# Kernel optimization log

Measured on AMD Instinct MI355X. Metric: run time of the kernel, lower is better.

Reference implementation:

```python
import jax, jax.numpy as jnp
import numpy as np
import math

B, N, C, H, DC = 1, 320, 128, 4, 32  # batch, residues, pair channels, heads, per-head dim


def setup_inputs() -> dict:
    key = jax.random.key(0)
    ks = jax.random.split(key, 8)
    s = lambda k, shape: jax.random.normal(k, shape, dtype=jnp.float32) * 0.02
    return {
        "x2d": jax.random.normal(ks[0], (B, N, N, C), dtype=jnp.float32),
        "mask": jnp.ones((B, N, N), dtype=jnp.float32),
        "ln_g": jnp.ones((C,), jnp.float32),
        "ln_b": jnp.zeros((C,), jnp.float32),
        "wq": s(ks[1], (C, H * DC)),
        "wk": s(ks[2], (C, H * DC)),
        "wv": s(ks[3], (C, H * DC)),
        "wb": s(ks[4], (C, H)),
        "wg": s(ks[5], (C, H * DC)),
        "bg": jnp.zeros((H * DC,), jnp.float32),
        "wo": s(ks[6], (H * DC, C)),
        "bo": jnp.zeros((C,), jnp.float32),
    }


def reference(x2d, mask, ln_g, ln_b, wq, wk, wv, wb, wg, bg, wo, bo):
    # ending_node = False -> no transpose
    # LayerNorm (torch uses biased variance, eps=1e-5)
    mu = x2d.mean(-1, keepdims=True)
    var = ((x2d - mu) ** 2).mean(-1, keepdims=True)
    xn = (x2d - mu) * jax.lax.rsqrt(var + 1e-5) * ln_g + ln_b  # [B,N,N,C]

    sh = xn.shape[:-1]  # (B, N, N)
    q = (xn @ wq).reshape(*sh, H, DC)
    k = (xn @ wk).reshape(*sh, H, DC)
    v = (xn @ wv).reshape(*sh, H, DC)

    scale = 1.0 / math.sqrt(DC)
    aff = jnp.einsum('bmihc,bmjhc->bmhij', q * scale, k)  # [B,N,H,N,N]

    # pair bias: [B,I,J,H] -> [B,1,H,I,J], broadcast over the row axis m
    bterm = jnp.einsum('bijc,ch->bhij', xn, wb)[:, None]
    mask_bias = (100000.0 * (mask - 1.0))[:, :, None, None, :]  # [B,N,1,1,N]

    weights = jax.nn.softmax(aff + bterm + mask_bias, axis=-1)

    g = jax.nn.sigmoid((xn @ wg + bg).reshape(*sh, H, DC))
    out = jnp.einsum('bmhqk,bmkhc->bmqhc', weights, v) * g  # [B,N,N,H,DC]
    out = out.reshape(*sh, H * DC) @ wo + bo  # [B,N,N,C]
    return out
```

## Files before the change

### kernel.cpp

```cpp
#include <hip/hip_runtime.h>
#include <hip/hip_bf16.h>

typedef __attribute__((ext_vector_type(8))) short bf16x8;
typedef __attribute__((ext_vector_type(4))) float f32x4;
typedef __attribute__((ext_vector_type(4))) unsigned short u16x4;

#define DEVI static __device__ __forceinline__

DEVI float bf2f(unsigned short u) {
    union { unsigned int ui; float f; } c; c.ui = ((unsigned int)u) << 16; return c.f;
}
DEVI unsigned short f2bf(float f) {
    union { float f; unsigned int ui; } c; c.f = f;
    unsigned int u = c.ui;
    u += 0x7FFFu + ((u >> 16) & 1u);
    return (unsigned short)(u >> 16);
}
DEVI unsigned int pk2bf(float a, float b) {
    union { __hip_bfloat162 h; unsigned int u; } c;
    c.h = __float22bfloat162_rn(make_float2(a, b));
    return c.u;
}

#define NRES 320
#define NN   102400
#define CCH  128
#define NPAD 328

#define LOG2E 1.4426950408889634f
#define QSCALE (0.17677669529663687f * 1.4426950408889634f)

__global__ __launch_bounds__(256) void k_ln_bias(
    const float* __restrict__ x2d, const float* __restrict__ ln_g,
    const float* __restrict__ ln_b, const float* __restrict__ wb,
    unsigned short* __restrict__ xn, float* __restrict__ bterm)
{
    int wave = threadIdx.x >> 6, lane = threadIdx.x & 63;
    int r = blockIdx.x * 4 + wave;
    int c0 = lane * 2;
    float2 x = *(const float2*)(x2d + (size_t)r * CCH + c0);
    float s = x.x + x.y, sq = x.x * x.x + x.y * x.y;
    #pragma unroll
    for (int m = 1; m < 64; m <<= 1) { s += __shfl_xor(s, m, 64); sq += __shfl_xor(sq, m, 64); }
    float mu = s * (1.0f / 128.0f);
    float var = sq * (1.0f / 128.0f) - mu * mu;
    float rstd = rsqrtf(var + 1e-5f);
    float xn0 = (x.x - mu) * rstd * ln_g[c0] + ln_b[c0];
    float xn1 = (x.y - mu) * rstd * ln_g[c0 + 1] + ln_b[c0 + 1];
    *(unsigned int*)(xn + (size_t)r * CCH + c0) = pk2bf(xn0, xn1);
    float4 w0 = *(const float4*)(wb + c0 * 4);
    float4 w1 = *(const float4*)(wb + c0 * 4 + 4);
    float b0 = xn0 * w0.x + xn1 * w1.x;
    float b1 = xn0 * w0.y + xn1 * w1.y;
    float b2 = xn0 * w0.z + xn1 * w1.z;
    float b3 = xn0 * w0.w + xn1 * w1.w;
    #pragma unroll
    for (int m = 1; m < 64; m <<= 1) {
        b0 += __shfl_xor(b0, m, 64); b1 += __shfl_xor(b1, m, 64);
        b2 += __shfl_xor(b2, m, 64); b3 += __shfl_xor(b3, m, 64);
    }
    if (lane == 0) {
        bterm[0 * NN + r] = b0 * LOG2E; bterm[1 * NN + r] = b1 * LOG2E;
        bterm[2 * NN + r] = b2 * LOG2E; bterm[3 * NN + r] = b3 * LOG2E;
    }
}

__global__ __launch_bounds__(256) void k_proj(
    const unsigned short* __restrict__ xn,
    const float* __restrict__ wq, const float* __restrict__ wk,
    const float* __restrict__ wv, const float* __restrict__ wg,
    const float* __restrict__ bg,
    unsigned short* __restrict__ qkvg)
{
    __shared__ unsigned short A[128][136];
    __shared__ unsigned short Bt[128][136];
    int m0 = blockIdx.x * 128;
    int nt = blockIdx.y;
    int t = threadIdx.x;
    const float* wsrc = (nt == 0) ? wq : (nt == 1) ? wk : (nt == 2) ? wv : wg;
    #pragma unroll
    for (int it = 0; it < 8; ++it) {
        int idx = it * 256 + t;
        int row = idx >> 4, chunk = idx & 15;
        *(bf16x8*)(&A[row][chunk * 8]) = *(const bf16x8*)(xn + (size_t)(m0 + row) * CCH + chunk * 8);
    }
    {
        int n = t & 127, p = t >> 7;
        const float* col = wsrc + n;
        #pragma unroll
        for (int q = 0; q < 8; ++q) {
            int k0 = p * 64 + q * 8;
            union { unsigned int u[4]; bf16x8 v; } pk;
            #pragma unroll
            for (int z = 0; z < 4; ++z)
                pk.u[z] = pk2bf(col[(size_t)(k0 + 2 * z) * 128], col[(size_t)(k0 + 2 * z + 1) * 128]);
            *(bf16x8*)(&Bt[n][k0]) = pk.v;
        }
    }
    __syncthreads();
    int wave = t >> 6, lane = t & 63;
    int wr = (wave >> 1) * 64, wc = (wave & 1) * 64;
    int li = lane & 15, lk = (lane >> 4) * 8;
    f32x4 acc[4][4] = {};
    #pragma unroll
    for (int kk = 0; kk < 4; ++kk) {
        bf16x8 af[4], bfr[4];
        #pragma unroll
        for (int i = 0; i < 4; ++i) af[i] = *(const bf16x8*)(&A[wr + i * 16 + li][kk * 32 + lk]);
        #pragma unroll
        for (int j = 0; j < 4; ++j) bfr[j] = *(const bf16x8*)(&Bt[wc + j * 16 + li][kk * 32 + lk]);
        __builtin_amdgcn_s_setprio(1);
        #pragma unroll
        for (int i = 0; i < 4; ++i)
            #pragma unroll
            for (int j = 0; j < 4; ++j)
                acc[i][j] = __builtin_amdgcn_mfma_f32_16x16x32_bf16(af[i], bfr[j], acc[i][j], 0, 0, 0);
        __builtin_amdgcn_s_setprio(0);
    }
    int rbase = (lane >> 4) * 4;
    bool isg = (nt == 3), isq = (nt == 0);
    #pragma unroll
    for (int i = 0; i < 4; ++i) {
        #pragma unroll
        for (int j = 0; j < 4; ++j) {
            int col = wc + j * 16 + li;
            int gcol = nt * 128 + col;
            #pragma unroll
            for (int r = 0; r < 4; ++r) {
                int grow = m0 + wr + i * 16 + rbase + r;
                float v = acc[i][j][r];
                if (isg) { v += bg[col]; v = 1.0f / (1.0f + __expf(-v)); }
                if (isq) v *= QSCALE;
                qkvg[(size_t)grow * 512 + gcol] = f2bf(v);
            }
        }
    }
}

__global__ __launch_bounds__(256) void k_attn(
    const unsigned short* __restrict__ qkvg,
    const float* __restrict__ bterm,
    const float* __restrict__ mask,
    unsigned short* __restrict__ opre)
{
    __shared__ unsigned short Kl[320][40];
    __shared__ unsigned short VT[32][NPAD];
    __shared__ float mb[320];
    int bid = blockIdx.x;
    int m = bid >> 2, h = bid & 3;
    int t = threadIdx.x;
    size_t base = (size_t)m * NRES * 512;
    for (int idx = t; idx < NRES * 4; idx += 256) {
        int row = idx >> 2, q = idx & 3;
        *(bf16x8*)(&Kl[row][q * 8]) =
            *(const bf16x8*)(qkvg + base + (size_t)row * 512 + 128 + h * 32 + q * 8);
    }
    {
        int dc = t & 31, jg = t >> 5;
        #pragma unroll 8
        for (int jj = 0; jj < 40; jj += 2) {
            int j = jg * 40 + jj;
            unsigned short v0 = qkvg[base + (size_t)j * 512 + 256 + h * 32 + dc];
            unsigned short v1 = qkvg[base + (size_t)(j + 1) * 512 + 256 + h * 32 + dc];
            *(unsigned int*)(&VT[dc][j]) = (unsigned int)v0 | ((unsigned int)v1 << 16);
        }
    }
    for (int j = t; j < NRES; j += 256) mb[j] = (100000.0f * LOG2E) * (mask[(size_t)m * NRES + j] - 1.0f);
    __syncthreads();

    int wave = t >> 6, lane = t & 63;
    int li = lane & 15, lg = lane >> 4;
    int selhi = lg >> 1;
    int srcA = li + ((lane & 16) << 1);
    int srcB = srcA + 16;
    for (int c = 0; c < 5; ++c) {
        int i = wave * 80 + c * 16 + li;
        size_t qrow = base + (size_t)i * 512;
        bf16x8 qf = *(const bf16x8*)(qkvg + qrow + h * 32 + lg * 8);
        const float* brow = bterm + (size_t)h * NN + (size_t)i * NRES;
        f32x4 z = {0.f, 0.f, 0.f, 0.f};
        float mrun = -3.0e38f, sum = 0.0f;
        f32x4 o0 = z, o1 = z;
        float4 bb0 = *(const float4*)(brow + lg * 4);
        float4 bb1 = *(const float4*)(brow + 16 + lg * 4);
        float4 bb2 = *(const float4*)(brow + 32 + lg * 4);
        float4 bb3 = *(const float4*)(brow + 48 + lg * 4);
        #pragma unroll 1
        for (int ph = 0; ph < 5; ++ph) {
            f32x4 st[4];
            #pragma unroll
            for (int jf = 0; jf < 4; ++jf) {
                bf16x8 kf = *(const bf16x8*)(&Kl[ph * 64 + jf * 16 + li][lg * 8]);
                st[jf] = __builtin_amdgcn_mfma_f32_16x16x32_bf16(kf, qf, z, 0, 0, 0);
            }
            float4 bn0, bn1, bn2, bn3;
            if (ph < 4) {
                const float* bnx = brow + (ph + 1) * 64 + lg * 4;
                bn0 = *(const float4*)(bnx);
                bn1 = *(const float4*)(bnx + 16);
                bn2 = *(const float4*)(bnx + 32);
                bn3 = *(const float4*)(bnx + 48);
            }
            float mx = mrun;
            #pragma unroll
            for (int jf = 0; jf < 4; ++jf) {
                int j0 = ph * 64 + jf * 16 + lg * 4;
                float4 mm = *(const float4*)(&mb[j0]);
                float4 bb = (jf == 0) ? bb0 : (jf == 1) ? bb1 : (jf == 2) ? bb2 : bb3;
                st[jf][0] += bb.x + mm.x;
                st[jf][1] += bb.y + mm.y;
                st[jf][2] += bb.z + mm.z;
                st[jf][3] += bb.w + mm.w;
                mx = fmaxf(mx, fmaxf(fmaxf(st[jf][0], st[jf][1]), fmaxf(st[jf][2], st[jf][3])));
            }
            mx = fmaxf(mx, __shfl_xor(mx, 16, 64));
            mx = fmaxf(mx, __shfl_xor(mx, 32, 64));
            if (ph) {
                float corr = __builtin_amdgcn_exp2f(mrun - mx);
                sum *= corr;
                #pragma unroll
                for (int r = 0; r < 4; ++r) { o0[r] *= corr; o1[r] *= corr; }
            }
            mrun = mx;
            #pragma unroll
            for (int w = 0; w < 2; ++w) {
                int jfA = w * 2, jfB = w * 2 + 1;
                float e0 = __builtin_amdgcn_exp2f(st[jfA][0] - mx);
                float e1 = __builtin_amdgcn_exp2f(st[jfA][1] - mx);
                float e2 = __builtin_amdgcn_exp2f(st[jfA][2] - mx);
                float e3 = __builtin_amdgcn_exp2f(st[jfA][3] - mx);
                float f0 = __builtin_amdgcn_exp2f(st[jfB][0] - mx);
                float f1 = __builtin_amdgcn_exp2f(st[jfB][1] - mx);
                float f2 = __builtin_amdgcn_exp2f(st[jfB][2] - mx);
                float f3 = __builtin_amdgcn_exp2f(st[jfB][3] - mx);
                sum += ((e0 + e1) + (e2 + e3)) + ((f0 + f1) + (f2 + f3));
                unsigned int q0 = pk2bf(e0, e1), q1 = pk2bf(e2, e3);
                unsigned int q2 = pk2bf(f0, f1), q3 = pk2bf(f2, f3);
                unsigned int t0 = __shfl((int)q0, srcA, 64), t2 = __shfl((int)q2, srcA, 64);
                unsigned int t1 = __shfl((int)q1, srcA, 64), t3 = __shfl((int)q3, srcA, 64);
                unsigned int u0 = __shfl((int)q0, srcB, 64), u2 = __shfl((int)q2, srcB, 64);
                unsigned int u1 = __shfl((int)q1, srcB, 64), u3 = __shfl((int)q3, srcB, 64);
                union { unsigned int u[4]; bf16x8 v; } pf;
                pf.u[0] = selhi ? t2 : t0;
                pf.u[1] = selhi ? t3 : t1;
                pf.u[2] = selhi ? u2 : u0;
                pf.u[3] = selhi ? u3 : u1;
                bf16x8 va = *(const bf16x8*)(&VT[li][ph * 64 + w * 32 + lg * 8]);
                bf16x8 vb = *(const bf16x8*)(&VT[16 + li][ph * 64 + w * 32 + lg * 8]);
                o0 = __builtin_amdgcn_mfma_f32_16x16x32_bf16(va, pf.v, o0, 0, 0, 0);
                o1 = __builtin_amdgcn_mfma_f32_16x16x32_bf16(vb, pf.v, o1, 0, 0, 0);
            }
            bb0 = bn0; bb1 = bn1; bb2 = bn2; bb3 = bn3;
        }
        sum += __shfl_xor(sum, 16, 64);
        sum += __shfl_xor(sum, 32, 64);
        float inv = 1.0f / sum;
        size_t orow = ((size_t)m * NRES + i) * CCH + h * 32;
        #pragma unroll
        for (int df = 0; df < 2; ++df) {
            f32x4 o = df ? o1 : o0;
            int dcb = df * 16 + lg * 4;
            u16x4 gv = *(const u16x4*)(qkvg + qrow + 384 + h * 32 + dcb);
            u16x4 ov;
            #pragma unroll
            for (int r = 0; r < 4; ++r) ov[r] = f2bf(o[r] * inv * bf2f(gv[r]));
            *(u16x4*)(opre + orow + dcb) = ov;
        }
    }
}

__global__ __launch_bounds__(256) void k_out(
    const unsigned short* __restrict__ opre, const float* __restrict__ wo,
    const float* __restrict__ bo, float* __restrict__ out)
{
    __shared__ unsigned short A[128][136];
    __shared__ unsigned short Bt[128][136];
    int m0 = blockIdx.x * 128;
    int t = threadIdx.x;
    #pragma unroll
    for (int it = 0; it < 8; ++it) {
        int idx = it * 256 + t;
        int row = idx >> 4, chunk = idx & 15;
        *(bf16x8*)(&A[row][chunk * 8]) = *(const bf16x8*)(opre + (size_t)(m0 + row) * CCH + chunk * 8);
    }
    {
        int n = t & 127, p = t >> 7;
        const float* col = wo + n;
        #pragma unroll
        for (int q = 0; q < 8; ++q) {
            int k0 = p * 64 + q * 8;
            union { unsigned int u[4]; bf16x8 v; } pk;
            #pragma unroll
            for (int z = 0; z < 4; ++z)
                pk.u[z] = pk2bf(col[(size_t)(k0 + 2 * z) * 128], col[(size_t)(k0 + 2 * z + 1) * 128]);
            *(bf16x8*)(&Bt[n][k0]) = pk.v;
        }
    }
    __syncthreads();
    int wave = t >> 6, lane = t & 63;
    int wr = (wave >> 1) * 64, wc = (wave & 1) * 64;
    int li = lane & 15, lk = (lane >> 4) * 8;
    f32x4 acc[4][4] = {};
    #pragma unroll
    for (int kk = 0; kk < 4; ++kk) {
        bf16x8 af[4], bfr[4];
        #pragma unroll
        for (int i = 0; i < 4; ++i) af[i] = *(const bf16x8*)(&A[wr + i * 16 + li][kk * 32 + lk]);
        #pragma unroll
        for (int j = 0; j < 4; ++j) bfr[j] = *(const bf16x8*)(&Bt[wc + j * 16 + li][kk * 32 + lk]);
        __builtin_amdgcn_s_setprio(1);
        #pragma unroll
        for (int i = 0; i < 4; ++i)
            #pragma unroll
            for (int j = 0; j < 4; ++j)
                acc[i][j] = __builtin_amdgcn_mfma_f32_16x16x32_bf16(af[i], bfr[j], acc[i][j], 0, 0, 0);
        __builtin_amdgcn_s_setprio(0);
    }
    int rbase = (lane >> 4) * 4;
    #pragma unroll
    for (int i = 0; i < 4; ++i) {
        #pragma unroll
        for (int j = 0; j < 4; ++j) {
            int col = wc + j * 16 + li;
            #pragma unroll
            for (int r = 0; r < 4; ++r) {
                int grow = m0 + wr + i * 16 + rbase + r;
                out[(size_t)grow * CCH + col] = acc[i][j][r] + bo[col];
            }
        }
    }
}

extern "C" void kernel_launch(void* const* d_in, const int* in_sizes, int n_in,
                              void* d_out, int out_size, void* d_ws, size_t ws_size,
                              hipStream_t stream) {
    const float* x2d  = (const float*)d_in[0];
    const float* mask = (const float*)d_in[1];
    const float* ln_g = (const float*)d_in[2];
    const float* ln_b = (const float*)d_in[3];
    const float* wq   = (const float*)d_in[4];
    const float* wk   = (const float*)d_in[5];
    const float* wv   = (const float*)d_in[6];
    const float* wb   = (const float*)d_in[7];
    const float* wg   = (const float*)d_in[8];
    const float* bg   = (const float*)d_in[9];
    const float* wo   = (const float*)d_in[10];
    const float* bo   = (const float*)d_in[11];
    float* out = (float*)d_out;

    char* ws = (char*)d_ws;
    unsigned short* xn    = (unsigned short*)ws;
    unsigned short* qkvg  = (unsigned short*)(ws + 26214400);
    float*          bterm = (float*)(ws + 26214400 + 104857600);
    unsigned short* opre  = xn;

    if (ws_size < (size_t)(26214400 + 104857600 + 1638400)) return;

    k_ln_bias<<<25600, 256, 0, stream>>>(x2d, ln_g, ln_b, wb, xn, bterm);
    k_proj<<<dim3(800, 4), 256, 0, stream>>>(xn, wq, wk, wv, wg, bg, qkvg);
    k_attn<<<1280, 256, 0, stream>>>(qkvg, bterm, mask, opre);
    k_out<<<800, 256, 0, stream>>>(opre, wo, bo, out);
}
```

Measured before the change: 211.7 us.

## Fuse LayerNorm into projection GEMM, add mask fast path, MFMA row sums

The LayerNorm+pair-bias kernel is merged into the projection kernel. Each block normalizes its 128 rows straight into shared memory and loops over the four weight matrices, so the bf16 xn round trip to global memory and one launch go away. In attention, a block-wide flag skips the mask-bias add when the whole mask row is ones. The softmax denominator now comes from an extra MFMA against a ones vector instead of scalar adds and shuffles. The trade-offs are one extra MFMA per tile and fewer, larger projection blocks (800 instead of 3200), which may reduce parallelism.

After: 249.0 us. 17.6% more time.

```diff
diff --git a/kernel.cpp b/kernel.cpp
--- a/kernel.cpp
+++ b/kernel.cpp
@@ -30,108 +30,122 @@
 #define LOG2E 1.4426950408889634f
 #define QSCALE (0.17677669529663687f * 1.4426950408889634f)
 
-__global__ __launch_bounds__(256) void k_ln_bias(
+__global__ __launch_bounds__(256) void k_projln(
     const float* __restrict__ x2d, const float* __restrict__ ln_g,
     const float* __restrict__ ln_b, const float* __restrict__ wb,
-    unsigned short* __restrict__ xn, float* __restrict__ bterm)
-{
-    int wave = threadIdx.x >> 6, lane = threadIdx.x & 63;
-    int r = blockIdx.x * 4 + wave;
-    int c0 = lane * 2;
-    float2 x = *(const float2*)(x2d + (size_t)r * CCH + c0);
-    float s = x.x + x.y, sq = x.x * x.x + x.y * x.y;
-    #pragma unroll
-    for (int m = 1; m < 64; m <<= 1) { s += __shfl_xor(s, m, 64); sq += __shfl_xor(sq, m, 64); }
-    float mu = s * (1.0f / 128.0f);
-    float var = sq * (1.0f / 128.0f) - mu * mu;
-    float rstd = rsqrtf(var + 1e-5f);
-    float xn0 = (x.x - mu) * rstd * ln_g[c0] + ln_b[c0];
-    float xn1 = (x.y - mu) * rstd * ln_g[c0 + 1] + ln_b[c0 + 1];
-    *(unsigned int*)(xn + (size_t)r * CCH + c0) = pk2bf(xn0, xn1);
-    float4 w0 = *(const float4*)(wb + c0 * 4);
-    float4 w1 = *(const float4*)(wb + c0 * 4 + 4);
-    float b0 = xn0 * w0.x + xn1 * w1.x;
-    float b1 = xn0 * w0.y + xn1 * w1.y;
-    float b2 = xn0 * w0.z + xn1 * w1.z;
-    float b3 = xn0 * w0.w + xn1 * w1.w;
-    #pragma unroll
-    for (int m = 1; m < 64; m <<= 1) {
-        b0 += __shfl_xor(b0, m, 64); b1 += __shfl_xor(b1, m, 64);
-        b2 += __shfl_xor(b2, m, 64); b3 += __shfl_xor(b3, m, 64);
-    }
-    if (lane == 0) {
-        bterm[0 * NN + r] = b0 * LOG2E; bterm[1 * NN + r] = b1 * LOG2E;
-        bterm[2 * NN + r] = b2 * LOG2E; bterm[3 * NN + r] = b3 * LOG2E;
-    }
-}
-
-__global__ __launch_bounds__(256) void k_proj(
-    const unsigned short* __restrict__ xn,
     const float* __restrict__ wq, const float* __restrict__ wk,
     const float* __restrict__ wv, const float* __restrict__ wg,
     const float* __restrict__ bg,
-    unsigned short* __restrict__ qkvg)
+    unsigned short* __restrict__ qkvg, float* __restrict__ bterm)
 {
     __shared__ unsigned short A[128][136];
     __shared__ unsigned short Bt[128][136];
     int m0 = blockIdx.x * 128;
-    int nt = blockIdx.y;
     int t = threadIdx.x;
-    const float* wsrc = (nt == 0) ? wq : (nt == 1) ? wk : (nt == 2) ? wv : wg;
-    #pragma unroll
-    for (int it = 0; it < 8; ++it) {
-        int idx = it * 256 + t;
-        int row = idx >> 4, chunk = idx & 15;
-        *(bf16x8*)(&A[row][chunk * 8]) = *(const bf16x8*)(xn + (size_t)(m0 + row) * CCH + chunk * 8);
-    }
-    {
-        int n = t & 127, p = t >> 7;
-        const float* col = wsrc + n;
-        #pragma unroll
-        for (int q = 0; q < 8; ++q) {
-            int k0 = p * 64 + q * 8;
-            union { unsigned int u[4]; bf16x8 v; } pk;
-            #pragma unroll
-            for (int z = 0; z < 4; ++z)
-                pk.u[z] = pk2bf(col[(size_t)(k0 + 2 * z) * 128], col[(size_t)(k0 + 2 * z + 1) * 128]);
-            *(bf16x8*)(&Bt[n][k0]) = pk.v;
-        }
-    }
-    __syncthreads();
+    int row = t >> 1, half = t & 1;
+    const float* xr = x2d + (size_t)(m0 + row) * CCH + half * 64;
+    float4 xv[16];
+    float s = 0.f, sq = 0.f;
+    #pragma unroll
+    for (int i = 0; i < 16; ++i) {
+        xv[i] = *(const float4*)(xr + i * 4);
+        s += (xv[i].x + xv[i].y) + (xv[i].z + xv[i].w);
+        sq += (xv[i].x * xv[i].x + xv[i].y * xv[i].y) + (xv[i].z * xv[i].z + xv[i].w * xv[i].w);
+    }
+    s += __shfl_xor(s, 1, 64); sq += __shfl_xor(sq, 1, 64);
+    float mu = s * (1.0f / 128.0f);
+    float var = sq * (1.0f / 128.0f) - mu * mu;
+    float rstd = rsqrtf(var + 1e-5f);
+    float bp0 = 0.f, bp1 = 0.f, bp2 = 0.f, bp3 = 0.f;
+    #pragma unroll
+    for (int g8 = 0; g8 < 8; ++g8) {
+        int c0 = half * 64 + g8 * 8;
+        float4 ga = *(const float4*)(ln_g + c0), gb = *(const float4*)(ln_g + c0 + 4);
+        float4 ba = *(const float4*)(ln_b + c0), bbv = *(const float4*)(ln_b + c0 + 4);
+        float4 a = xv[g8 * 2], b = xv[g8 * 2 + 1];
+        float xf[8];
+        xf[0] = (a.x - mu) * rstd * ga.x + ba.x;
+        xf[1] = (a.y - mu) * rstd * ga.y + ba.y;
+        xf[2] = (a.z - mu) * rstd * ga.z + ba.z;
+        xf[3] = (a.w - mu) * rstd * ga.w + ba.w;
+        xf[4] = (b.x - mu) * rstd * gb.x + bbv.x;
+        xf[5] = (b.y - mu) * rstd * gb.y + bbv.y;
+        xf[6] = (b.z - mu) * rstd * gb.z + bbv.z;
+        xf[7] = (b.w - mu) * rstd * gb.w + bbv.w;
+        #pragma unroll
+        for (int z = 0; z < 8; ++z) {
+            float4 w = *(const float4*)(wb + (c0 + z) * 4);
+            bp0 += xf[z] * w.x; bp1 += xf[z] * w.y;
+            bp2 += xf[z] * w.z; bp3 += xf[z] * w.w;
+        }
+        union { unsigned int u[4]; bf16x8 v; } pk;
+        #pragma unroll
+        for (int z = 0; z < 4; ++z) pk.u[z] = pk2bf(xf[2 * z], xf[2 * z + 1]);
+        *(bf16x8*)(&A[row][c0]) = pk.v;
+    }
+    bp0 += __shfl_xor(bp0, 1, 64); bp1 += __shfl_xor(bp1, 1, 64);
+    bp2 += __shfl_xor(bp2, 1, 64); bp3 += __shfl_xor(bp3, 1, 64);
+    if (!half) {
+        int r = m0 + row;
+        bterm[0 * NN + r] = bp0 * LOG2E; bterm[1 * NN + r] = bp1 * LOG2E;
+        bterm[2 * NN + r] = bp2 * LOG2E; bterm[3 * NN + r] = bp3 * LOG2E;
+    }
     int wave = t >> 6, lane = t & 63;
     int wr = (wave >> 1) * 64, wc = (wave & 1) * 64;
     int li = lane & 15, lk = (lane >> 4) * 8;
-    f32x4 acc[4][4] = {};
-    #pragma unroll
-    for (int kk = 0; kk < 4; ++kk) {
-        bf16x8 af[4], bfr[4];
-        #pragma unroll
-        for (int i = 0; i < 4; ++i) af[i] = *(const bf16x8*)(&A[wr + i * 16 + li][kk * 32 + lk]);
-        #pragma unroll
-        for (int j = 0; j < 4; ++j) bfr[j] = *(const bf16x8*)(&Bt[wc + j * 16 + li][kk * 32 + lk]);
-        __builtin_amdgcn_s_setprio(1);
-        #pragma unroll
-        for (int i = 0; i < 4; ++i)
-            #pragma unroll
-            for (int j = 0; j < 4; ++j)
-                acc[i][j] = __builtin_amdgcn_mfma_f32_16x16x32_bf16(af[i], bfr[j], acc[i][j], 0, 0, 0);
-        __builtin_amdgcn_s_setprio(0);
-    }
     int rbase = (lane >> 4) * 4;
-    bool isg = (nt == 3), isq = (nt == 0);
-    #pragma unroll
-    for (int i = 0; i < 4; ++i) {
-        #pragma unroll
-        for (int j = 0; j < 4; ++j) {
-            int col = wc + j * 16 + li;
-            int gcol = nt * 128 + col;
-            #pragma unroll
-            for (int r = 0; r < 4; ++r) {
-                int grow = m0 + wr + i * 16 + rbase + r;
-                float v = acc[i][j][r];
-                if (isg) { v += bg[col]; v = 1.0f / (1.0f + __expf(-v)); }
-                if (isq) v *= QSCALE;
-                qkvg[(size_t)grow * 512 + gcol] = f2bf(v);
+    const float* Ws[4] = { wq, wk, wv, wg };
+    for (int nt = 0; nt < 4; ++nt) {
+        if (nt) __syncthreads();
+        const float* wsrc = Ws[nt];
+        {
+            int n = t & 127, p = t >> 7;
+            const float* col = wsrc + n;
+            #pragma unroll
+            for (int q = 0; q < 4; ++q) {
+                int k0 = p * 64 + q * 16;
+                union { unsigned int u[4]; bf16x8 v; } pka, pkb;
+                #pragma unroll
+                for (int z = 0; z < 4; ++z) {
+                    pka.u[z] = pk2bf(col[(size_t)(k0 + 2 * z) * 128], col[(size_t)(k0 + 2 * z + 1) * 128]);
+                    pkb.u[z] = pk2bf(col[(size_t)(k0 + 8 + 2 * z) * 128], col[(size_t)(k0 + 9 + 2 * z) * 128]);
+                }
+                *(bf16x8*)(&Bt[n][k0]) = pka.v;
+                *(bf16x8*)(&Bt[n][k0 + 8]) = pkb.v;
+            }
+        }
+        __syncthreads();
+        f32x4 acc[4][4] = {};
+        #pragma unroll
+        for (int kk = 0; kk < 4; ++kk) {
+            bf16x8 af[4], bfr[4];
+            #pragma unroll
+            for (int i = 0; i < 4; ++i) af[i] = *(const bf16x8*)(&A[wr + i * 16 + li][kk * 32 + lk]);
+            #pragma unroll
+            for (int j = 0; j < 4; ++j) bfr[j] = *(const bf16x8*)(&Bt[wc + j * 16 + li][kk * 32 + lk]);
+            __builtin_amdgcn_s_setprio(1);
+            #pragma unroll
+            for (int i = 0; i < 4; ++i)
+                #pragma unroll
+                for (int j = 0; j < 4; ++j)
+                    acc[i][j] = __builtin_amdgcn_mfma_f32_16x16x32_bf16(af[i], bfr[j], acc[i][j], 0, 0, 0);
+            __builtin_amdgcn_s_setprio(0);
+        }
+        bool isg = (nt == 3), isq = (nt == 0);
+        #pragma unroll
+        for (int i = 0; i < 4; ++i) {
+            #pragma unroll
+            for (int j = 0; j < 4; ++j) {
+                int col = wc + j * 16 + li;
+                int gcol = nt * 128 + col;
+                #pragma unroll
+                for (int r = 0; r < 4; ++r) {
+                    int grow = m0 + wr + i * 16 + rbase + r;
+                    float v = acc[i][j][r];
+                    if (isg) { v += bg[col]; v = 1.0f / (1.0f + __expf(-v)); }
+                    if (isq) v *= QSCALE;
+                    qkvg[(size_t)grow * 512 + gcol] = f2bf(v);
+                }
             }
         }
     }
@@ -146,10 +160,13 @@
     __shared__ unsigned short Kl[320][40];
     __shared__ unsigned short VT[32][NPAD];
     __shared__ float mb[320];
+    __shared__ int allone;
     int bid = blockIdx.x;
     int m = bid >> 2, h = bid & 3;
     int t = threadIdx.x;
     size_t base = (size_t)m * NRES * 512;
+    if (t == 0) allone = 1;
+    __syncthreads();
     for (int idx = t; idx < NRES * 4; idx += 256) {
         int row = idx >> 2, q = idx & 3;
         *(bf16x8*)(&Kl[row][q * 8]) =
@@ -165,22 +182,30 @@
             *(unsigned int*)(&VT[dc][j]) = (unsigned int)v0 | ((unsigned int)v1 << 16);
         }
     }
-    for (int j = t; j < NRES; j += 256) mb[j] = (100000.0f * LOG2E) * (mask[(size_t)m * NRES + j] - 1.0f);
+    for (int j = t; j < NRES; j += 256) {
+        float mmv = (100000.0f * LOG2E) * (mask[(size_t)m * NRES + j] - 1.0f);
+        mb[j] = mmv;
+        if (mmv != 0.0f) allone = 0;
+    }
     __syncthreads();
+    bool nomask = (allone != 0);
 
     int wave = t >> 6, lane = t & 63;
     int li = lane & 15, lg = lane >> 4;
     int selhi = lg >> 1;
     int srcA = li + ((lane & 16) << 1);
     int srcB = srcA + 16;
+    bf16x8 onef;
+    #pragma unroll
+    for (int z = 0; z < 8; ++z) onef[z] = (short)0x3F80;
     for (int c = 0; c < 5; ++c) {
         int i = wave * 80 + c * 16 + li;
         size_t qrow = base + (size_t)i * 512;
         bf16x8 qf = *(const bf16x8*)(qkvg + qrow + h * 32 + lg * 8);
         const float* brow = bterm + (size_t)h * NN + (size_t)i * NRES;
         f32x4 z = {0.f, 0.f, 0.f, 0.f};
-        float mrun = -3.0e38f, sum = 0.0f;
-        f32x4 o0 = z, o1 = z;
+        float mrun = -3.0e38f;
+        f32x4 o0 = z, o1 = z, o2 = z;
         float4 bb0 = *(const float4*)(brow + lg * 4);
         float4 bb1 = *(const float4*)(brow + 16 + lg * 4);
         float4 bb2 = *(const float4*)(brow + 32 + lg * 4);
@@ -202,24 +227,36 @@
                 bn3 = *(const float4*)(bnx + 48);
             }
             float mx = mrun;
-            #pragma unroll
-            for (int jf = 0; jf < 4; ++jf) {
-                int j0 = ph * 64 + jf * 16 + lg * 4;
-                float4 mm = *(const float4*)(&mb[j0]);
-                float4 bb = (jf == 0) ? bb0 : (jf == 1) ? bb1 : (jf == 2) ? bb2 : bb3;
-                st[jf][0] += bb.x + mm.x;
-                st[jf][1] += bb.y + mm.y;
-                st[jf][2] += bb.z + mm.z;
-                st[jf][3] += bb.w + mm.w;
-                mx = fmaxf(mx, fmaxf(fmaxf(st[jf][0], st[jf][1]), fmaxf(st[jf][2], st[jf][3])));
+            if (nomask) {
+                #pragma unroll
+                for (int jf = 0; jf < 4; ++jf) {
+                    float4 bb = (jf == 0) ? bb0 : (jf == 1) ? bb1 : (jf == 2) ? bb2 : bb3;
+                    st[jf][0] += bb.x;
+                    st[jf][1] += bb.y;
+                    st[jf][2] += bb.z;
+                    st[jf][3] += bb.w;
+                    mx = fmaxf(mx, fmaxf(fmaxf(st[jf][0], st[jf][1]), fmaxf(st[jf][2], st[jf][3])));
+                }
+            } else {
+                #pragma unroll
+                for (int jf = 0; jf < 4; ++jf) {
+                    int j0 = ph * 64 + jf * 16 + lg * 4;
+                    float4 mm = *(const float4*)(&mb[j0]);
+                    float4 bb = (jf == 0) ? bb0 : (jf == 1) ? bb1 : (jf == 2) ? bb2 : bb3;
+                    st[jf][0] += bb.x + mm.x;
+                    st[jf][1] += bb.y + mm.y;
+                    st[jf][2] += bb.z + mm.z;
+                    st[jf][3] += bb.w + mm.w;
+                    mx = fmaxf(mx, fmaxf(fmaxf(st[jf][0], st[jf][1]), fmaxf(st[jf][2], st[jf][3])));
+                }
             }
             mx = fmaxf(mx, __shfl_xor(mx, 16, 64));
             mx = fmaxf(mx, __shfl_xor(mx, 32, 64));
             if (ph) {
                 float corr = __builtin_amdgcn_exp2f(mrun - mx);
-                sum *= corr;
                 #pragma unroll
                 for (int r = 0; r < 4; ++r) { o0[r] *= corr; o1[r] *= corr; }
+                o2[0] *= corr;
             }
             mrun = mx;
             #pragma unroll
@@ -233,7 +270,6 @@
                 float f1 = __builtin_amdgcn_exp2f(st[jfB][1] - mx);
                 float f2 = __builtin_amdgcn_exp2f(st[jfB][2] - mx);
                 float f3 = __builtin_amdgcn_exp2f(st[jfB][3] - mx);
-                sum += ((e0 + e1) + (e2 + e3)) + ((f0 + f1) + (f2 + f3));
                 unsigned int q0 = pk2bf(e0, e1), q1 = pk2bf(e2, e3);
                 unsigned int q2 = pk2bf(f0, f1), q3 = pk2bf(f2, f3);
                 unsigned int t0 = __shfl((int)q0, srcA, 64), t2 = __shfl((int)q2, srcA, 64);
@@ -249,12 +285,11 @@
                 bf16x8 vb = *(const bf16x8*)(&VT[16 + li][ph * 64 + w * 32 + lg * 8]);
                 o0 = __builtin_amdgcn_mfma_f32_16x16x32_bf16(va, pf.v, o0, 0, 0, 0);
                 o1 = __builtin_amdgcn_mfma_f32_16x16x32_bf16(vb, pf.v, o1, 0, 0, 0);
+                o2 = __builtin_amdgcn_mfma_f32_16x16x32_bf16(onef, pf.v, o2, 0, 0, 0);
             }
             bb0 = bn0; bb1 = bn1; bb2 = bn2; bb3 = bn3;
         }
-        sum += __shfl_xor(sum, 16, 64);
-        sum += __shfl_xor(sum, 32, 64);
-        float inv = 1.0f / sum;
+        float inv = 1.0f / o2[0];
         size_t orow = ((size_t)m * NRES + i) * CCH + h * 32;
         #pragma unroll
         for (int df = 0; df < 2; ++df) {
@@ -349,15 +384,13 @@
     float* out = (float*)d_out;
 
     char* ws = (char*)d_ws;
-    unsigned short* xn    = (unsigned short*)ws;
+    unsigned short* opre  = (unsigned short*)ws;
     unsigned short* qkvg  = (unsigned short*)(ws + 26214400);
     float*          bterm = (float*)(ws + 26214400 + 104857600);
-    unsigned short* opre  = xn;
 
     if (ws_size < (size_t)(26214400 + 104857600 + 1638400)) return;
 
-    k_ln_bias<<<25600, 256, 0, stream>>>(x2d, ln_g, ln_b, wb, xn, bterm);
-    k_proj<<<dim3(800, 4), 256, 0, stream>>>(xn, wq, wk, wv, wg, bg, qkvg);
+    k_projln<<<800, 256, 0, stream>>>(x2d, ln_g, ln_b, wb, wq, wk, wv, wg, bg, qkvg, bterm);
     k_attn<<<1280, 256, 0, stream>>>(qkvg, bterm, mask, opre);
     k_out<<<800, 256, 0, stream>>>(opre, wo, bo, out);
 }
```
